# Kernel optimization log

Hardware: AMD Instinct MI355X
Metric: run time of the kernel (lower is better)

## Reference

```python
import jax, jax.numpy as jnp
import numpy as np

B, K, H, W = 16, 32, 28, 28   # batch, set size, image h, image w
HID, OUT = 64, 64             # hid_dim, out_dim
NOPS = 8                      # permutation-equivariant 3->3 pool/broadcast basis ops


def setup_inputs() -> dict:
    key = jax.random.key(0)
    ks = jax.random.split(key, 8)
    def p(k, shape, fan_in):
        return jax.random.normal(k, shape, jnp.float32) / np.float32(np.sqrt(fan_in))
    return dict(
        x=jax.random.normal(ks[0], (B, K, H, W), jnp.float32),
        conv1_w=p(ks[1], (32, 1, 3, 3), 9),
        conv1_b=jnp.zeros((32,), jnp.float32),
        conv2_w=p(ks[2], (64, 32, 3, 3), 32 * 9),
        conv2_b=jnp.zeros((64,), jnp.float32),
        fc_w=p(ks[3], (HID, 64 * 7 * 7), 64 * 7 * 7),
        fc_b=jnp.zeros((HID,), jnp.float32),
        eq_w=p(ks[4], (HID, OUT, NOPS), HID * NOPS),
        eq_b=jnp.zeros((OUT,), jnp.float32),
        out_w=p(ks[5], (1, OUT), OUT),
        out_b=jnp.zeros((1,), jnp.float32),
    )


def _conv2d(x, w, b):
    y = jax.lax.conv_general_dilated(x, w, (1, 1), 'SAME',
                                     dimension_numbers=('NCHW', 'OIHW', 'NCHW'))
    return y + b[None, :, None, None]


def _maxpool2(x):
    return jax.lax.reduce_window(x, -jnp.inf, jax.lax.max,
                                 (1, 1, 2, 2), (1, 1, 2, 2), 'VALID')


def _forward(x, conv1_w, conv1_b, conv2_w, conv2_b, fc_w, fc_b, eq_w, eq_b, out_w, out_b):
    # --- BasicConvNet embed: (B*K, 1, H, W) -> (B*K, HID) ---
    x1 = x.reshape(B * K, 1, H, W)
    h1 = _maxpool2(jax.nn.relu(_conv2d(x1, conv1_w, conv1_b)))   # (B*K, 32, 14, 14)
    h2 = _maxpool2(jax.nn.relu(_conv2d(h1, conv2_w, conv2_b)))   # (B*K, 64, 7, 7)
    feat = jax.nn.relu(h2.reshape(B * K, -1) @ fc_w.T + fc_b)    # (B*K, HID)
    x4 = feat.reshape(B, K, HID)

    # --- triple outer product: (B, HID, K, K, K), no contracted index ---
    x5 = jnp.einsum('bid,bjd,bkd->bdijk', x4, x4, x4)

    # --- SetEq3to3: 8 equivariant pool/broadcast basis ops, contracted with eq_w[d,e,o].
    # Contract each pooled tensor with its slice of eq_w BEFORE broadcasting (same math,
    # avoids materializing 8 full (B,d,K,K,K) op tensors). ---
    m_i  = x5.mean(2)           # (B, d, j, k)
    m_j  = x5.mean(3)           # (B, d, i, k)
    m_k  = x5.mean(4)           # (B, d, i, j)
    m_ij = m_i.mean(2)          # (B, d, k)
    m_ik = m_i.mean(3)          # (B, d, j)
    m_jk = m_j.mean(3)          # (B, d, i)
    m_all = m_ij.mean(2)        # (B, d)

    x6 = (jnp.einsum('bdijk,de->beijk', x5, eq_w[:, :, 0])
          + jnp.einsum('bdjk,de->bejk', m_i, eq_w[:, :, 1])[:, :, None, :, :]
          + jnp.einsum('bdik,de->beik', m_j, eq_w[:, :, 2])[:, :, :, None, :]
          + jnp.einsum('bdij,de->beij', m_k, eq_w[:, :, 3])[:, :, :, :, None]
          + jnp.einsum('bdk,de->bek', m_ij, eq_w[:, :, 4])[:, :, None, None, :]
          + jnp.einsum('bdj,de->bej', m_ik, eq_w[:, :, 5])[:, :, None, :, None]
          + jnp.einsum('bdi,de->bei', m_jk, eq_w[:, :, 6])[:, :, :, None, None]
          + jnp.einsum('bd,de->be', m_all, eq_w[:, :, 7])[:, :, None, None, None]
          + eq_b[None, :, None, None, None])          # (B, OUT, K, K, K)

    # permute to channels-last, relu, pool over (i,j,k), relu, final linear
    x7 = jax.nn.relu(x6.transpose(0, 2, 3, 4, 1))     # (B, K, K, K, OUT)
    x8 = x7.mean(axis=(1, 2, 3))                      # (B, OUT)
    x9 = jax.nn.relu(x8)
    # dropout_prob = 0 -> identity
    return x9 @ out_w.T + out_b                       # (B, 1)


def reference(x, conv1_w, conv1_b, conv2_w, conv2_b, fc_w, fc_b, eq_w, eq_b, out_w, out_b):
    return _forward(x, conv1_w, conv1_b, conv2_w, conv2_b, fc_w, fc_b,
                    eq_w, eq_b, out_w, out_b)
```

## Files before the change

kernel.cpp:

```cpp
#include <hip/hip_runtime.h>


typedef __attribute__((ext_vector_type(8))) short short8;
typedef __attribute__((ext_vector_type(4))) float f32x4;

__device__ __forceinline__ f32x4 mfma_bf16(short8 a, short8 b, f32x4 c) {
  return __builtin_amdgcn_mfma_f32_16x16x32_bf16(a, b, c, 0, 0, 0);
}

__device__ __forceinline__ unsigned short f2bs(float f) {
  unsigned int u = __float_as_uint(f);
  unsigned int r = u + 0x7fffu + ((u >> 16) & 1u);
  return (unsigned short)(r >> 16);
}
__device__ __forceinline__ unsigned int pk2(float x, float y) {
  return (unsigned int)f2bs(x) | ((unsigned int)f2bs(y) << 16);
}
__device__ __forceinline__ void stb4(short* p, float4 v) {
  *(unsigned int*)(p)     = pk2(v.x, v.y);
  *(unsigned int*)(p + 2) = pk2(v.z, v.w);
}

__global__ __launch_bounds__(256) void k1_conv1(const float* __restrict__ x,
    const float* __restrict__ w, const float* __restrict__ bias,
    float* __restrict__ h1,
    const float* __restrict__ eqw, float* __restrict__ Wt,
    const float* __restrict__ fcw, short* __restrict__ fcwb) {
  const int n = blockIdx.x, t = threadIdx.x;
  if (n >= 512) {
    if (n < 520) {
      const int m = n - 512;
      for (int idx = t; idx < 4096; idx += 256) {
        int e = idx >> 6, d = idx & 63;
        Wt[m*4096 + idx] = eqw[d*512 + e*8 + m];
      }
    } else {
      int base = (n - 520)*12544 + t;
      for (int q = 0; q < 49; ++q) {
        int idx = base + q*256;
        fcwb[idx] = (short)f2bs(fcw[idx]);
      }
    }
    return;
  }
  __shared__ float si[30*30];
  __shared__ float sw[32*9];
  __shared__ float sb[32];
  for (int idx = t; idx < 900; idx += 256) si[idx] = 0.f;
  for (int idx = t; idx < 288; idx += 256) sw[idx] = w[idx];
  if (t < 32) sb[t] = bias[t];
  __syncthreads();
  for (int idx = t; idx < 784; idx += 256) {
    int y = idx / 28, xx = idx - y*28;
    si[(y+1)*30 + xx + 1] = x[n*784 + idx];
  }
  __syncthreads();
  for (int item = t; item < 6272; item += 256) {
    int c = item / 196, rem = item - c*196;
    int py = rem / 14, px = rem - py*14;
    float pt[4][4];
#pragma unroll
    for (int r = 0; r < 4; ++r)
#pragma unroll
      for (int q = 0; q < 4; ++q)
        pt[r][q] = si[(2*py + r)*30 + 2*px + q];
    const float* wc = &sw[c*9];
    float w0=wc[0], w1=wc[1], w2=wc[2], w3=wc[3], w4=wc[4], w5=wc[5], w6=wc[6], w7=wc[7], w8=wc[8];
    float bb = sb[c];
    float best = 0.f;
#pragma unroll
    for (int a = 0; a < 2; ++a)
#pragma unroll
      for (int b2 = 0; b2 < 2; ++b2) {
        float v = bb
          + w0*pt[a+0][b2+0] + w1*pt[a+0][b2+1] + w2*pt[a+0][b2+2]
          + w3*pt[a+1][b2+0] + w4*pt[a+1][b2+1] + w5*pt[a+1][b2+2]
          + w6*pt[a+2][b2+0] + w7*pt[a+2][b2+1] + w8*pt[a+2][b2+2];
        best = fmaxf(best, v);
      }
    h1[n*6272 + item] = best;
  }
}

__global__ __launch_bounds__(256, 2) void k2_mfma(const float* __restrict__ h1,
    const float* __restrict__ w, const float* __restrict__ bias,
    short* __restrict__ h2b) {
  __shared__ __align__(16) short inT[16*18*40];
  const int n = blockIdx.x, t = threadIdx.x;
  const int wv = t >> 6, l = t & 63, quad = l >> 4, col = l & 15;

  unsigned int* zp = (unsigned int*)inT;
  for (int idx = t; idx < 16*18*20; idx += 256) zp[idx] = 0u;

  const int c_out = wv*16 + col;
  float w72[72];
  {
    const float4* src = (const float4*)(w + c_out*288 + quad*72);
#pragma unroll
    for (int q = 0; q < 18; ++q) {
      float4 v = src[q];
      w72[q*4+0] = v.x; w72[q*4+1] = v.y; w72[q*4+2] = v.z; w72[q*4+3] = v.w;
    }
  }
  union SU { short8 v; unsigned int u[4]; };
  short8 Bq[9];
#pragma unroll
  for (int dd = 0; dd < 9; ++dd) {
    SU b;
#pragma unroll
    for (int q = 0; q < 4; ++q)
      b.u[q] = pk2(w72[(2*q)*9 + dd], w72[(2*q+1)*9 + dd]);
    Bq[dd] = b.v;
  }
  const float bb = bias[c_out];
  __syncthreads();

  for (int idx = t; idx < 6272; idx += 256) {
    int c = idx / 196, rem = idx - c*196, y = rem / 14, x = rem - y*14;
    inT[(y+1)*720 + (x+1)*40 + c] = (short)f2bs(h1[n*6272 + idx]);
  }
  __syncthreads();

  for (int p = 0; p < 7; ++p) {
    short8 Ar[4][3];
#pragma unroll
    for (int rr = 0; rr < 4; ++rr)
#pragma unroll
      for (int dx = 0; dx < 3; ++dx)
        Ar[rr][dx] = *(const short8*)&inT[(2*p + rr)*720 + (col + dx)*40 + quad*8];
    f32x4 a0 = {0.f,0.f,0.f,0.f}, a1 = {0.f,0.f,0.f,0.f};
#pragma unroll
    for (int dy = 0; dy < 3; ++dy)
#pragma unroll
      for (int dx = 0; dx < 3; ++dx) {
        a0 = mfma_bf16(Ar[dy][dx],     Bq[dy*3 + dx], a0);
        a1 = mfma_bf16(Ar[dy + 1][dx], Bq[dy*3 + dx], a1);
      }
#pragma unroll
    for (int a = 0; a < 2; ++a) {
      int px = quad*2 + a;
      if (px < 7) {
        float m0 = fmaxf(fmaxf(a0[2*a], a0[2*a + 1]), fmaxf(a1[2*a], a1[2*a + 1]));
        h2b[n*3136 + c_out*49 + p*7 + px] = (short)f2bs(fmaxf(m0 + bb, 0.f));
      }
    }
  }
}

__global__ __launch_bounds__(256) void k3_mfma(const short* __restrict__ h2b,
    const short* __restrict__ fcwb, float* __restrict__ part) {
  const int blk = blockIdx.x, kp = blockIdx.y, t = threadIdx.x;
  const int w = t >> 6, l = t & 63, quad = l >> 4, col = l & 15;
  const int mt = w & 1, nh = w >> 1;
  const int img = blk*32 + mt*16 + col;
  const short* Ap = h2b + img*3136 + kp*224 + quad*8;
  const short* B0 = fcwb + (nh*32 + col)*3136 + kp*224 + quad*8;
  const short* B1 = fcwb + (nh*32 + 16 + col)*3136 + kp*224 + quad*8;
  f32x4 acc0 = {0.f,0.f,0.f,0.f}, acc1 = {0.f,0.f,0.f,0.f};
#pragma unroll
  for (int q = 0; q < 7; ++q) {
    short8 A  = *(const short8*)(Ap + q*32);
    short8 b0 = *(const short8*)(B0 + q*32);
    short8 b1 = *(const short8*)(B1 + q*32);
    acc0 = mfma_bf16(A, b0, acc0);
    acc1 = mfma_bf16(A, b1, acc1);
  }
  const int e0 = nh*32 + col, e1 = e0 + 16;
  const int base = blk*32 + mt*16 + quad*4;
  float* dst = part + kp*32768;
#pragma unroll
  for (int r = 0; r < 4; ++r) {
    dst[(base + r)*64 + e0] = acc0[r];
    dst[(base + r)*64 + e1] = acc1[r];
  }
}

__global__ __launch_bounds__(256) void k4_prep(const float* __restrict__ part,
    const float* __restrict__ fb, const float* __restrict__ Wt,
    const float* __restrict__ eqb, float* __restrict__ feat,
    float* __restrict__ s, float* __restrict__ t7c, float* __restrict__ x8) {
  __shared__ __align__(16) float sf[2048];
  __shared__ float ss[64];
  const int b = blockIdx.x, t = threadIdx.x;
  for (int v4 = t; v4 < 512; v4 += 256) {
    float4 a = {0.f, 0.f, 0.f, 0.f};
#pragma unroll
    for (int kp = 0; kp < 14; ++kp) {
      float4 p = *(const float4*)&part[kp*32768 + b*2048 + v4*4];
      a.x += p.x; a.y += p.y; a.z += p.z; a.w += p.w;
    }
    float4 fbv = *(const float4*)&fb[(v4*4) & 63];
    float4 r;
    r.x = fmaxf(a.x + fbv.x, 0.f);
    r.y = fmaxf(a.y + fbv.y, 0.f);
    r.z = fmaxf(a.z + fbv.z, 0.f);
    r.w = fmaxf(a.w + fbv.w, 0.f);
    *(float4*)&sf[v4*4] = r;
    *(float4*)&feat[b*2048 + v4*4] = r;
  }
  __syncthreads();
  if (t < 64) {
    float a = 0.f;
    for (int i = 0; i < 32; ++i) a += sf[i*64 + t];
    a *= (1.f/32.f);
    s[b*64 + t] = a;
    ss[t] = a;
  }
  __syncthreads();
  if (t < 64) {
    const float* W7 = Wt + 7*4096 + t*64;
    float t7 = 0.f;
    for (int d = 0; d < 64; ++d) {
      float sv = ss[d];
      t7 += sv*sv*sv * W7[d];
    }
    t7c[b*64 + t] = t7 + eqb[t];
    x8[b*64 + t] = 0.f;
  }
}

__global__ __launch_bounds__(256, 2) void k5_mfma(const float* __restrict__ feat,
    const float* __restrict__ s_, const float* __restrict__ Wt,
    const float* __restrict__ t7c, float* __restrict__ x8) {
  __shared__ __align__(16) float Fm[32*68];
  __shared__ __align__(16) float FI[64];
  __shared__ __align__(16) float SV[64];
  __shared__ __align__(16) float C0[64];
  __shared__ float C0P[128];
  __shared__ float KCf[32*68];
  __shared__ float JCf[32*68];
  __shared__ float RED[256];
  __shared__ __align__(16) short Fb[32*72];
  __shared__ __align__(16) short QPb[64*72];
  __shared__ __align__(16) short G2b[64*72];
  __shared__ __align__(16) short G3b[64*72];

  const int i = blockIdx.x, b = blockIdx.y, t = threadIdx.x;
  const int w = t >> 6, l = t & 63, quad = l >> 4, col = l & 15;

  for (int idx = t; idx < 2048; idx += 256) {
    int r = idx >> 6, d = idx & 63;
    float v = feat[b*2048 + idx];
    Fm[r*68 + d] = v;
    Fb[r*72 + d] = (short)f2bs(v);
  }
  if (t < 64) { FI[t] = feat[b*2048 + i*64 + t]; SV[t] = s_[b*64 + t]; }
  __syncthreads();

  {
    const int e = t >> 2, dbase = (t & 3) * 16;
    const float* W0 = Wt + 0*4096 + e*64;
    const float* W1 = Wt + 1*4096 + e*64;
    const float* W2 = Wt + 2*4096 + e*64;
    const float* W3 = Wt + 3*4096 + e*64;
    const float* W4 = Wt + 4*4096 + e*64;
    const float* W5 = Wt + 5*4096 + e*64;
#pragma unroll
    for (int q = 0; q < 4; ++q) {
      int off = dbase + q*4;
      float4 fi4 = *(const float4*)&FI[off];
      float4 sv4 = *(const float4*)&SV[off];
      float4 w0 = *(const float4*)&W0[off];
      float4 w1 = *(const float4*)&W1[off];
      float4 w2 = *(const float4*)&W2[off];
      float4 w3 = *(const float4*)&W3[off];
      float4 w4 = *(const float4*)&W4[off];
      float4 w5 = *(const float4*)&W5[off];
      float4 qp = fi4*w0 + sv4*w1;
      float4 g2 = sv4*(fi4*w2 + sv4*w4);
      float4 g3 = sv4*(fi4*w3 + sv4*w5);
      stb4(&QPb[e*72 + off], qp);
      stb4(&G2b[e*72 + off], g2);
      stb4(&G3b[e*72 + off], g3);
    }
  }
  if (t < 128) {
    int e = t & 63, dh = t >> 6;
    const float* W6 = Wt + 6*4096 + e*64 + dh*32;
    const float* fip = FI + dh*32;
    const float* svp = SV + dh*32;
    float a = 0.f;
#pragma unroll
    for (int dd = 0; dd < 32; ++dd) {
      float sd = svp[dd];
      a += sd*sd*fip[dd]*W6[dd];
    }
    C0P[dh*64 + e] = a;
  }
  __syncthreads();

  if (w < 2) {
    const short* G = w ? G3b : G2b;
    float* DST = w ? JCf : KCf;
    short8 Bf[4][2];
#pragma unroll
    for (int n = 0; n < 4; ++n)
#pragma unroll
      for (int s2 = 0; s2 < 2; ++s2)
        Bf[n][s2] = *(const short8*)&G[(n*16 + col)*72 + s2*32 + quad*8];
#pragma unroll
    for (int m = 0; m < 2; ++m) {
      short8 A0 = *(const short8*)&Fb[(m*16 + col)*72 + quad*8];
      short8 A1 = *(const short8*)&Fb[(m*16 + col)*72 + 32 + quad*8];
#pragma unroll
      for (int n = 0; n < 4; ++n) {
        f32x4 z = {0.f, 0.f, 0.f, 0.f};
        f32x4 ac = mfma_bf16(A1, Bf[n][1], mfma_bf16(A0, Bf[n][0], z));
#pragma unroll
        for (int r = 0; r < 4; ++r)
          DST[(m*16 + quad*4 + r)*68 + n*16 + col] = ac[r];
      }
    }
  } else if (w == 2) {
    C0[l] = C0P[l] + C0P[64 + l] + t7c[b*64 + l];
  }
  __syncthreads();

  float c0v[4];
#pragma unroll
  for (int n = 0; n < 4; ++n) c0v[n] = C0[n*16 + col];
  float jcq[8][4];
#pragma unroll
  for (int jj = 0; jj < 8; ++jj)
#pragma unroll
    for (int n = 0; n < 4; ++n)
      jcq[jj][n] = JCf[(w*8 + jj)*68 + n*16 + col] + c0v[n];
  float kcv[2][4][4];
#pragma unroll
  for (int kb2 = 0; kb2 < 2; ++kb2)
#pragma unroll
    for (int r = 0; r < 4; ++r)
#pragma unroll
      for (int n = 0; n < 4; ++n)
        kcv[kb2][r][n] = KCf[(kb2*16 + quad*4 + r)*68 + n*16 + col];
  short8 Bq[4][2];
#pragma unroll
  for (int n = 0; n < 4; ++n)
#pragma unroll
    for (int s2 = 0; s2 < 2; ++s2)
      Bq[n][s2] = *(const short8*)&QPb[(n*16 + col)*72 + s2*32 + quad*8];

  float sum[4] = {0.f, 0.f, 0.f, 0.f};
  union SU { short8 v; unsigned int u[4]; };

#pragma unroll
  for (int mi = 0; mi < 16; ++mi) {
    const int jj = mi >> 1, kb2 = mi & 1;
    const float* fj = &Fm[(w*8 + jj)*68 + quad*8];
    const float* fk = &Fm[(kb2*16 + col)*68 + quad*8];
    float4 ja0 = *(const float4*)(fj);
    float4 ja1 = *(const float4*)(fj + 4);
    float4 jb0 = *(const float4*)(fj + 32);
    float4 jb1 = *(const float4*)(fj + 36);
    float4 ka0 = *(const float4*)(fk);
    float4 ka1 = *(const float4*)(fk + 4);
    float4 kb0 = *(const float4*)(fk + 32);
    float4 kb1 = *(const float4*)(fk + 36);
    SU A0, A1;
    A0.u[0] = pk2(ja0.x*ka0.x, ja0.y*ka0.y);
    A0.u[1] = pk2(ja0.z*ka0.z, ja0.w*ka0.w);
    A0.u[2] = pk2(ja1.x*ka1.x, ja1.y*ka1.y);
    A0.u[3] = pk2(ja1.z*ka1.z, ja1.w*ka1.w);
    A1.u[0] = pk2(jb0.x*kb0.x, jb0.y*kb0.y);
    A1.u[1] = pk2(jb0.z*kb0.z, jb0.w*kb0.w);
    A1.u[2] = pk2(jb1.x*kb1.x, jb1.y*kb1.y);
    A1.u[3] = pk2(jb1.z*kb1.z, jb1.w*kb1.w);
    f32x4 ac[4];
#pragma unroll
    for (int n = 0; n < 4; ++n) {
      f32x4 z = {0.f, 0.f, 0.f, 0.f};
      ac[n] = mfma_bf16(A1.v, Bq[n][1], mfma_bf16(A0.v, Bq[n][0], z));
    }
#pragma unroll
    for (int n = 0; n < 4; ++n)
#pragma unroll
      for (int r = 0; r < 4; ++r) {
        float v = ac[n][r] + kcv[kb2][r][n] + jcq[jj][n];
        sum[n] += fmaxf(v, 0.f);
      }
  }

#pragma unroll
  for (int n = 0; n < 4; ++n) {
    float v = sum[n];
    v += __shfl_xor(v, 16, 64);
    v += __shfl_xor(v, 32, 64);
    if (l < 16) RED[w*64 + n*16 + l] = v;
  }
  __syncthreads();
  if (t < 64) {
    float tot = RED[t] + RED[64 + t] + RED[128 + t] + RED[192 + t];
    atomicAdd(&x8[b*64 + t], tot);
  }
}

__global__ __launch_bounds__(64) void k6_out(const float* __restrict__ x8,
    const float* __restrict__ ow, const float* __restrict__ ob,
    float* __restrict__ out) {
  const int bb = blockIdx.x, t = threadIdx.x;
  float v = fmaxf(x8[bb*64 + t] * (1.f/32768.f), 0.f) * ow[t];
#pragma unroll
  for (int off = 32; off > 0; off >>= 1) v += __shfl_down(v, off, 64);
  if (t == 0) out[bb] = v + ob[0];
}

extern "C" void kernel_launch(void* const* d_in, const int* in_sizes, int n_in,
                              void* d_out, int out_size, void* d_ws, size_t ws_size,
                              hipStream_t stream) {
  const float* x   = (const float*)d_in[0];
  const float* c1w = (const float*)d_in[1];
  const float* c1b = (const float*)d_in[2];
  const float* c2w = (const float*)d_in[3];
  const float* c2b = (const float*)d_in[4];
  const float* fcw = (const float*)d_in[5];
  const float* fcb = (const float*)d_in[6];
  const float* eqw = (const float*)d_in[7];
  const float* eqb = (const float*)d_in[8];
  const float* ow  = (const float*)d_in[9];
  const float* ob  = (const float*)d_in[10];
  float* out = (float*)d_out;

  float* ws   = (float*)d_ws;
  float* h1   = ws;
  short* h2b  = (short*)(h1 + 512*6272);
  float* feat = (float*)(h2b + 512*3136);
  float* s    = feat + 512*64;
  float* t7c  = s + 1024;
  float* x8   = t7c + 1024;
  float* Wt   = x8 + 1024;
  short* fcwb = (short*)(Wt + 32768);
  float* part = (float*)(fcwb + 200704);

  hipLaunchKernelGGL(k1_conv1, dim3(536), dim3(256), 0, stream,
                     x, c1w, c1b, h1, eqw, Wt, fcw, fcwb);
  hipLaunchKernelGGL(k2_mfma,  dim3(512), dim3(256), 0, stream, h1, c2w, c2b, h2b);
  hipLaunchKernelGGL(k3_mfma,  dim3(16, 14), dim3(256), 0, stream, h2b, fcwb, part);
  hipLaunchKernelGGL(k4_prep,  dim3(16),  dim3(256), 0, stream,
                     part, fcb, Wt, eqb, feat, s, t7c, x8);
  hipLaunchKernelGGL(k5_mfma,  dim3(32, 16), dim3(256), 0, stream, feat, s, Wt, t7c, x8);
  hipLaunchKernelGGL(k6_out,   dim3(16),  dim3(64),  0, stream, x8, ow, ob, out);
}
```

Measured before the change: 137.5 us.

## Store conv1 output as channels-last bf16 and hoist k-side loads in k5

Conv1 now writes its pooled output as bf16 in position-major, channel-minor order, so conv2 can fill its shared tile with 16-byte vector copies instead of scalar fp32 loads followed by conversion. This halves the intermediate traffic between the two kernels. The pack helper now uses the HIP bfloat162 intrinsic. In k5, the k-side feature vectors are loaded into registers once before the loop, and the loop is restructured over jj, which adds register pressure.

```diff
diff --git a/kernel.cpp b/kernel.cpp
--- a/kernel.cpp
+++ b/kernel.cpp
@@ -1,4 +1,5 @@
 #include <hip/hip_runtime.h>
+#include <hip/hip_bf16.h>
 
 
 typedef __attribute__((ext_vector_type(8))) short short8;
@@ -14,7 +15,9 @@
   return (unsigned short)(r >> 16);
 }
 __device__ __forceinline__ unsigned int pk2(float x, float y) {
-  return (unsigned int)f2bs(x) | ((unsigned int)f2bs(y) << 16);
+  union { __hip_bfloat162 h; unsigned int u; } cv;
+  cv.h = __float22bfloat162_rn(make_float2(x, y));
+  return cv.u;
 }
 __device__ __forceinline__ void stb4(short* p, float4 v) {
   *(unsigned int*)(p)     = pk2(v.x, v.y);
@@ -23,7 +26,7 @@
 
 __global__ __launch_bounds__(256) void k1_conv1(const float* __restrict__ x,
     const float* __restrict__ w, const float* __restrict__ bias,
-    float* __restrict__ h1,
+    short* __restrict__ h1b,
     const float* __restrict__ eqw, float* __restrict__ Wt,
     const float* __restrict__ fcw, short* __restrict__ fcwb) {
   const int n = blockIdx.x, t = threadIdx.x;
@@ -55,9 +58,9 @@
     si[(y+1)*30 + xx + 1] = x[n*784 + idx];
   }
   __syncthreads();
-  for (int item = t; item < 6272; item += 256) {
-    int c = item / 196, rem = item - c*196;
-    int py = rem / 14, px = rem - py*14;
+  for (int idx = t; idx < 6272; idx += 256) {
+    int pos = idx >> 5, c = idx & 31;
+    int py = pos / 14, px = pos - py*14;
     float pt[4][4];
 #pragma unroll
     for (int r = 0; r < 4; ++r)
@@ -78,11 +81,11 @@
           + w6*pt[a+2][b2+0] + w7*pt[a+2][b2+1] + w8*pt[a+2][b2+2];
         best = fmaxf(best, v);
       }
-    h1[n*6272 + item] = best;
-  }
-}
-
-__global__ __launch_bounds__(256, 2) void k2_mfma(const float* __restrict__ h1,
+    h1b[n*6272 + idx] = (short)f2bs(best);
+  }
+}
+
+__global__ __launch_bounds__(256, 2) void k2_mfma(const short* __restrict__ h1b,
     const float* __restrict__ w, const float* __restrict__ bias,
     short* __restrict__ h2b) {
   __shared__ __align__(16) short inT[16*18*40];
@@ -115,9 +118,14 @@
   const float bb = bias[c_out];
   __syncthreads();
 
-  for (int idx = t; idx < 6272; idx += 256) {
-    int c = idx / 196, rem = idx - c*196, y = rem / 14, x = rem - y*14;
-    inT[(y+1)*720 + (x+1)*40 + c] = (short)f2bs(h1[n*6272 + idx]);
+  {
+    const uint4* src = (const uint4*)(h1b + n*6272);
+    for (int idx = t; idx < 784; idx += 256) {
+      uint4 v = src[idx];
+      int pos = idx >> 2, cb = (idx & 3) * 8;
+      int y = pos / 14, xx = pos - y*14;
+      *(uint4*)&inT[(y+1)*720 + (xx+1)*40 + cb] = v;
+    }
   }
   __syncthreads();
 
@@ -340,44 +348,53 @@
     for (int s2 = 0; s2 < 2; ++s2)
       Bq[n][s2] = *(const short8*)&QPb[(n*16 + col)*72 + s2*32 + quad*8];
 
+  float4 fkv[2][4];
+#pragma unroll
+  for (int kb2 = 0; kb2 < 2; ++kb2) {
+    const float* fk = &Fm[(kb2*16 + col)*68 + quad*8];
+    fkv[kb2][0] = *(const float4*)(fk);
+    fkv[kb2][1] = *(const float4*)(fk + 4);
+    fkv[kb2][2] = *(const float4*)(fk + 32);
+    fkv[kb2][3] = *(const float4*)(fk + 36);
+  }
+
   float sum[4] = {0.f, 0.f, 0.f, 0.f};
   union SU { short8 v; unsigned int u[4]; };
 
 #pragma unroll
-  for (int mi = 0; mi < 16; ++mi) {
-    const int jj = mi >> 1, kb2 = mi & 1;
+  for (int jj = 0; jj < 8; ++jj) {
     const float* fj = &Fm[(w*8 + jj)*68 + quad*8];
-    const float* fk = &Fm[(kb2*16 + col)*68 + quad*8];
-    float4 ja0 = *(const float4*)(fj);
-    float4 ja1 = *(const float4*)(fj + 4);
-    float4 jb0 = *(const float4*)(fj + 32);
-    float4 jb1 = *(const float4*)(fj + 36);
-    float4 ka0 = *(const float4*)(fk);
-    float4 ka1 = *(const float4*)(fk + 4);
-    float4 kb0 = *(const float4*)(fk + 32);
-    float4 kb1 = *(const float4*)(fk + 36);
-    SU A0, A1;
-    A0.u[0] = pk2(ja0.x*ka0.x, ja0.y*ka0.y);
-    A0.u[1] = pk2(ja0.z*ka0.z, ja0.w*ka0.w);
-    A0.u[2] = pk2(ja1.x*ka1.x, ja1.y*ka1.y);
-    A0.u[3] = pk2(ja1.z*ka1.z, ja1.w*ka1.w);
-    A1.u[0] = pk2(jb0.x*kb0.x, jb0.y*kb0.y);
-    A1.u[1] = pk2(jb0.z*kb0.z, jb0.w*kb0.w);
-    A1.u[2] = pk2(jb1.x*kb1.x, jb1.y*kb1.y);
-    A1.u[3] = pk2(jb1.z*kb1.z, jb1.w*kb1.w);
-    f32x4 ac[4];
-#pragma unroll
-    for (int n = 0; n < 4; ++n) {
-      f32x4 z = {0.f, 0.f, 0.f, 0.f};
-      ac[n] = mfma_bf16(A1.v, Bq[n][1], mfma_bf16(A0.v, Bq[n][0], z));
-    }
-#pragma unroll
-    for (int n = 0; n < 4; ++n)
-#pragma unroll
-      for (int r = 0; r < 4; ++r) {
-        float v = ac[n][r] + kcv[kb2][r][n] + jcq[jj][n];
-        sum[n] += fmaxf(v, 0.f);
-      }
+    float4 j0 = *(const float4*)(fj);
+    float4 j1 = *(const float4*)(fj + 4);
+    float4 j2 = *(const float4*)(fj + 32);
+    float4 j3 = *(const float4*)(fj + 36);
+#pragma unroll
+    for (int kb2 = 0; kb2 < 2; ++kb2) {
+      float4 k0 = fkv[kb2][0], k1 = fkv[kb2][1];
+      float4 k2v = fkv[kb2][2], k3v = fkv[kb2][3];
+      SU A0, A1;
+      A0.u[0] = pk2(j0.x*k0.x, j0.y*k0.y);
+      A0.u[1] = pk2(j0.z*k0.z, j0.w*k0.w);
+      A0.u[2] = pk2(j1.x*k1.x, j1.y*k1.y);
+      A0.u[3] = pk2(j1.z*k1.z, j1.w*k1.w);
+      A1.u[0] = pk2(j2.x*k2v.x, j2.y*k2v.y);
+      A1.u[1] = pk2(j2.z*k2v.z, j2.w*k2v.w);
+      A1.u[2] = pk2(j3.x*k3v.x, j3.y*k3v.y);
+      A1.u[3] = pk2(j3.z*k3v.z, j3.w*k3v.w);
+      f32x4 ac[4];
+#pragma unroll
+      for (int n = 0; n < 4; ++n) {
+        f32x4 z = {0.f, 0.f, 0.f, 0.f};
+        ac[n] = mfma_bf16(A1.v, Bq[n][1], mfma_bf16(A0.v, Bq[n][0], z));
+      }
+#pragma unroll
+      for (int n = 0; n < 4; ++n)
+#pragma unroll
+        for (int r = 0; r < 4; ++r) {
+          float v = ac[n][r] + kcv[kb2][r][n] + jcq[jj][n];
+          sum[n] += fmaxf(v, 0.f);
+        }
+    }
   }
 
 #pragma unroll
@@ -420,9 +437,8 @@
   const float* ob  = (const float*)d_in[10];
   float* out = (float*)d_out;
 
-  float* ws   = (float*)d_ws;
-  float* h1   = ws;
-  short* h2b  = (short*)(h1 + 512*6272);
+  short* h1b  = (short*)d_ws;
+  short* h2b  = h1b + 512*6272;
   float* feat = (float*)(h2b + 512*3136);
   float* s    = feat + 512*64;
   float* t7c  = s + 1024;
@@ -432,8 +448,8 @@
   float* part = (float*)(fcwb + 200704);
 
   hipLaunchKernelGGL(k1_conv1, dim3(536), dim3(256), 0, stream,
-                     x, c1w, c1b, h1, eqw, Wt, fcw, fcwb);
-  hipLaunchKernelGGL(k2_mfma,  dim3(512), dim3(256), 0, stream, h1, c2w, c2b, h2b);
+                     x, c1w, c1b, h1b, eqw, Wt, fcw, fcwb);
+  hipLaunchKernelGGL(k2_mfma,  dim3(512), dim3(256), 0, stream, h1b, c2w, c2b, h2b);
   hipLaunchKernelGGL(k3_mfma,  dim3(16, 14), dim3(256), 0, stream, h2b, fcwb, part);
   hipLaunchKernelGGL(k4_prep,  dim3(16),  dim3(256), 0, stream,
                      part, fcb, Wt, eqb, feat, s, t7c, x8);
```

New measurement: 131.5 us. 4.4% less time.
